# Performance work log

Hardware: AMD Instinct MI355X
Metric: run time of the kernel (lower is better)

The kernel has to match this reference:

```python
import jax, jax.numpy as jnp
import numpy as np

VOC, EDIM, HDIM, SSZ, SDIM, SDEPTH, PAD = 32000, 256, 256, 128, 128, 2, 0
N, BSZ = 64, 32
T = 2 * N - 1  # 127
N_ACTS = 2  # push, pop


def _linear(key, out_d, in_d):
    k1, k2 = jax.random.split(key)
    return (jax.random.normal(k1, (out_d, in_d), jnp.float32) * 0.02,
            jax.random.normal(k2, (out_d,), jnp.float32) * 0.02)


def setup_inputs() -> dict:
    key = jax.random.key(0)
    ks = jax.random.split(key, 9)
    emb_W = jax.random.normal(ks[0], (VOC, EDIM), jnp.float32) * 0.02
    emb_W = emb_W.at[PAD].set(0.0)  # padding_idx row is zero in torch
    W_e2h, b_e2h = _linear(ks[1], HDIM, EDIM)
    W_s2h, b_s2h = _linear(ks[2], HDIM, SDIM * SDEPTH)
    W_h2h, b_h2h = _linear(ks[3], HDIM, HDIM)
    W_h2i, b_h2i = _linear(ks[4], N_ACTS + 1, HDIM)
    W_h2s, b_h2s = _linear(ks[5], SDIM, HDIM)
    W_s2u, b_s2u = _linear(ks[6], SDIM, SDIM * SDEPTH)
    empty_elem = jax.random.normal(ks[7], (1, SDIM), jnp.float32) * 0.02
    inputs = jax.random.randint(ks[8], (N, BSZ), 0, VOC)
    return dict(inputs=inputs, emb_W=emb_W, W_e2h=W_e2h, b_e2h=b_e2h,
                W_s2h=W_s2h, b_s2h=b_s2h, W_h2h=W_h2h, b_h2h=b_h2h,
                W_h2i=W_h2i, b_h2i=b_h2i, W_h2s=W_h2s, b_h2s=b_h2s,
                W_s2u=W_s2u, b_s2u=b_s2u, empty_elem=empty_elem)


def _srnn(inputs, emb_W, W_e2h, b_e2h, W_s2h, b_s2h, W_h2h, b_h2h,
          W_h2i, b_h2i, W_h2s, b_h2s, W_s2u, b_s2u, empty_elem):
    bsz = inputs.shape[1]
    embs = emb_W[inputs]                                        # [N, bsz, edim]
    pads = jnp.broadcast_to(emb_W[PAD], (T - N, bsz, EDIM))     # padded tail
    buf0 = jnp.concatenate([embs, pads], axis=0)                # [T, bsz, edim]
    hid0 = jnp.zeros((bsz, HDIM), jnp.float32)
    stack0 = jnp.broadcast_to(empty_elem, (bsz, SSZ, SDIM))

    def step(carry, t):
        hid, stack, buf = carry
        tops = stack[:, :SDEPTH, :].reshape(bsz, SDEPTH * SDIM)
        inp = buf[t]                                            # [bsz, edim]
        ihid = inp @ W_e2h.T + b_e2h + tops @ W_s2h.T + b_s2h
        hid = jax.nn.relu(hid @ W_h2h.T + b_h2h + ihid)
        inst = ihid @ W_h2i.T + b_h2i                           # [bsz, 3]
        act = jax.nn.softmax(inst[:, :N_ACTS], axis=-1)
        gamma = 1.0 + jnp.log1p(jnp.exp(inst[:, N_ACTS:]))      # [bsz, 1]
        a = act ** gamma
        a = a / (jnp.sum(a, axis=-1, keepdims=True) + 1e-16)    # sharpened acts
        p_push, p_pop = a[:, :1], a[:, 1:]                      # [bsz, 1]
        # buffer update: pop shifts the whole buffer down one slot along time
        buf_pop = jnp.concatenate([jnp.zeros_like(buf[:1]), buf[:-1]], axis=0)
        buf = p_push[None] * buf + p_pop[None] * buf_pop        # [1,bsz,1] bcast
        push_val = jax.nn.relu(hid @ W_h2s.T + b_h2s)           # [bsz, sdim]
        u_val = jax.nn.relu(tops @ W_s2u.T + b_s2u)             # [bsz, sdim]
        z = jnp.zeros((bsz, 1, SDIM), jnp.float32)
        # W_push (shift down by 1) as an index roll
        stack_push = jnp.concatenate([z, stack[:, :-1, :]], axis=1)
        stack_push = stack_push.at[:, 0, :].add(push_val)
        # W_pop = shift up by SDEPTH, then W_push = shift down by 1
        up = jnp.concatenate([stack[:, SDEPTH:, :],
                              jnp.zeros((bsz, SDEPTH, SDIM), jnp.float32)], axis=1)
        stack_pop = jnp.concatenate([z, up[:, :-1, :]], axis=1)
        stack_pop = stack_pop.at[:, 0, :].add(u_val)
        stack_pop = stack_pop.at[:, SSZ - SDEPTH + 1:, :].add(empty_elem[0])
        stack = p_push[:, :, None] * stack_push + p_pop[:, :, None] * stack_pop
        return (hid, stack, buf), (hid, a, stack[:, 0, :])

    (hid, stack, _), (outputs, acts, top_elems) = jax.lax.scan(
        step, (hid0, stack0, buf0), jnp.arange(T))
    return outputs, hid, stack, acts, top_elems


def reference(inputs, emb_W, W_e2h, b_e2h, W_s2h, b_s2h, W_h2h, b_h2h,
              W_h2i, b_h2i, W_h2s, b_h2s, W_s2u, b_s2u, empty_elem):
    return _srnn(inputs, emb_W, W_e2h, b_e2h, W_s2h, b_s2h, W_h2h, b_h2h,
                 W_h2i, b_h2i, W_h2s, b_h2s, W_s2u, b_s2u, empty_elem)
```

## Files before the change

kernel.cpp:

```cpp
#include <hip/hip_runtime.h>
#include <stdint.h>
#include <math.h>


#define T_STEPS 127

#define OUT_OFF   0
#define HID_OFF   1040384
#define STACK_OFF 1048576
#define ACTS_OFF  1572864
#define TE_OFF    1580992

#define WB_OFF 16384
#define E2H_OFF_U 131072

typedef _Float16 h2 __attribute__((ext_vector_type(2)));

__device__ __forceinline__ unsigned packh2(float a, float b){
  h2 v; v.x = (_Float16)a; v.y = (_Float16)b;
  return __builtin_bit_cast(unsigned, v);
}
__device__ __forceinline__ float h2loF(unsigned u){ h2 v = __builtin_bit_cast(h2,u); return (float)v.x; }
__device__ __forceinline__ float h2hiF(unsigned u){ h2 v = __builtin_bit_cast(h2,u); return (float)v.y; }

#if __has_builtin(__builtin_amdgcn_fdot2)
__device__ __forceinline__ float fdot2(unsigned a, unsigned b, float c){
  return __builtin_amdgcn_fdot2(__builtin_bit_cast(h2,a), __builtin_bit_cast(h2,b), c, false);
}
#else
__device__ __forceinline__ float fdot2(unsigned a, unsigned b, float c){
  return c + h2loF(a)*h2loF(b) + h2hiF(a)*h2hiF(b);
}
#endif

#if __has_builtin(__builtin_amdgcn_exp2f)
#define EXP2F(x) __builtin_amdgcn_exp2f(x)
#else
#define EXP2F(x) exp2f(x)
#endif
#if __has_builtin(__builtin_amdgcn_logf)
#define LOG2F(x) __builtin_amdgcn_logf(x)
#else
#define LOG2F(x) log2f(x)
#endif
#if __has_builtin(__builtin_amdgcn_rcpf)
#define RCPF(x) __builtin_amdgcn_rcpf(x)
#else
#define RCPF(x) (1.f/(x))
#endif

#define DPP_XOR1 0xB1
#define DPP_XOR2 0x4E
#define DPP_HM   0x141
#define DPP_RM   0x140
template<int CTRL>
__device__ __forceinline__ float dppadd(float v){
  int s = __builtin_amdgcn_update_dpp(0, __builtin_bit_cast(int, v), CTRL, 0xF, 0xF, true);
  return v + __builtin_bit_cast(float, s);
}

#define BAR() asm volatile("s_waitcnt lgkmcnt(0)\n\ts_barrier" ::: "memory")

#define CHOFF(u) (12*((u)>>3) + ((u)&7))

__global__ void prep_pack(const float* __restrict__ We2h, const float* __restrict__ Ws2h,
                          const float* __restrict__ Wh2h, const float* __restrict__ Wh2s,
                          const float* __restrict__ Ws2u, uint4* __restrict__ out4){
  int gid = blockIdx.x*256 + threadIdx.x;
  const float* src;
  if (gid < 16384){
    int i = gid >> 10, t_ = gid & 1023;
    const float* S = (t_ < 512) ? Ws2h : Wh2h;
    int r = t_ & 511, jp = r >> 2, ks = r & 3;
    int j = 2*jp + (i >> 3);
    int k0 = ks*64 + (i & 7)*8;
    src = S + j*256 + k0;
  } else if (gid < 24576){
    int l = gid - 16384;
    int i = l >> 10, t_ = l & 1023;
    const float* S = (t_ < 512) ? Wh2s : Ws2u;
    int tt = t_ & 511;
    int j  = 2*(tt >> 3) + (i >> 2);
    int k0 = (tt & 7)*32 + (i & 3)*8;
    src = S + j*256 + k0;
  } else {
    int l = gid - 24576;
    int i8 = l >> 8, j = l & 255;
    src = We2h + j*256 + i8*8;
  }
  uint4 r4;
  r4.x = packh2(src[0], src[1]); r4.y = packh2(src[2], src[3]);
  r4.z = packh2(src[4], src[5]); r4.w = packh2(src[6], src[7]);
  out4[gid] = r4;
}

__global__ void prep_e2h(const int* __restrict__ inputs, const float* __restrict__ embW,
                         const uint4* __restrict__ w04, unsigned* __restrict__ e2hpk){
  __shared__ float emb[8][256];
  int tid = threadIdx.x;
  int r2 = blockIdx.x >> 3, bg = blockIdx.x & 7;
  for (int q=0;q<8;q++){
    int rr = q >> 2, bb = q & 3;
    int tok = inputs[(2*r2+rr)*32 + bg*4+bb];
    emb[q][tid] = embW[tok*256 + tid];
  }
  __syncthreads();
  float acc[8] = {0.f,0.f,0.f,0.f,0.f,0.f,0.f,0.f};
  for (int i8=0;i8<32;i8++){
    uint4 u = w04[i8*256 + tid];
    unsigned uu[4] = {u.x,u.y,u.z,u.w};
    #pragma unroll
    for (int c=0;c<4;c++){
      float lo = h2loF(uu[c]), hi = h2hiF(uu[c]);
      int k = i8*8 + c*2;
      #pragma unroll
      for (int q=0;q<8;q++)
        acc[q] += emb[q][k]*lo + emb[q][k+1]*hi;
    }
  }
  int base = (bg*4)*8192 + r2*256 + tid;
  #pragma unroll
  for (int bb=0;bb<4;bb++)
    e2hpk[base + bb*8192] = packh2(acc[bb], acc[4+bb]);
}

#define GEMV_B(SRC, Y0, Y1) \
  { const uint4* cA0_ = (const uint4*)((SRC) + 24*kB); \
    uint4 A0_ = cA0_[0], A1_ = cA0_[1]; \
    const uint4* cA1_ = (const uint4*)((SRC) + 24*kB + 12); \
    uint4 A2_ = cA1_[0], A3_ = cA1_[1]; \
    Y0=fdot2(A0_.x,wBr[0].x,Y0); Y0=fdot2(A0_.y,wBr[0].y,Y0); Y0=fdot2(A0_.z,wBr[0].z,Y0); Y0=fdot2(A0_.w,wBr[0].w,Y0); \
    Y0=fdot2(A1_.x,wBr[1].x,Y0); Y0=fdot2(A1_.y,wBr[1].y,Y0); Y0=fdot2(A1_.z,wBr[1].z,Y0); Y0=fdot2(A1_.w,wBr[1].w,Y0); \
    Y0=fdot2(A2_.x,wBr[2].x,Y0); Y0=fdot2(A2_.y,wBr[2].y,Y0); Y0=fdot2(A2_.z,wBr[2].z,Y0); Y0=fdot2(A2_.w,wBr[2].w,Y0); \
    Y0=fdot2(A3_.x,wBr[3].x,Y0); Y0=fdot2(A3_.y,wBr[3].y,Y0); Y0=fdot2(A3_.z,wBr[3].z,Y0); Y0=fdot2(A3_.w,wBr[3].w,Y0); \
    Y1=fdot2(A0_.x,wBr[4].x,Y1); Y1=fdot2(A0_.y,wBr[4].y,Y1); Y1=fdot2(A0_.z,wBr[4].z,Y1); Y1=fdot2(A0_.w,wBr[4].w,Y1); \
    Y1=fdot2(A1_.x,wBr[5].x,Y1); Y1=fdot2(A1_.y,wBr[5].y,Y1); Y1=fdot2(A1_.z,wBr[5].z,Y1); Y1=fdot2(A1_.w,wBr[5].w,Y1); \
    Y1=fdot2(A2_.x,wBr[6].x,Y1); Y1=fdot2(A2_.y,wBr[6].y,Y1); Y1=fdot2(A2_.z,wBr[6].z,Y1); Y1=fdot2(A2_.w,wBr[6].w,Y1); \
    Y1=fdot2(A3_.x,wBr[7].x,Y1); Y1=fdot2(A3_.y,wBr[7].y,Y1); Y1=fdot2(A3_.z,wBr[7].z,Y1); Y1=fdot2(A3_.w,wBr[7].w,Y1); \
    Y0 = dppadd<DPP_XOR1>(Y0); Y0 = dppadd<DPP_XOR2>(Y0); Y0 = dppadd<DPP_HM>(Y0); \
    Y1 = dppadd<DPP_XOR1>(Y1); Y1 = dppadd<DPP_XOR2>(Y1); Y1 = dppadd<DPP_HM>(Y1); }

__global__ __attribute__((amdgpu_flat_work_group_size(1024,1024), amdgpu_waves_per_eu(4,4)))
void srnn_main(const uint4* __restrict__ ws4, const unsigned* __restrict__ wsu,
               const float* __restrict__ b_e2h, const float* __restrict__ b_s2h,
               const float* __restrict__ b_h2h, const float* __restrict__ Wh2i,
               const float* __restrict__ b_h2i, const float* __restrict__ b_h2s,
               const float* __restrict__ b_s2u, const float* __restrict__ empty_el,
               float* __restrict__ out)
{
  __shared__ __align__(16) float    stk_s[128*128];
  __shared__ __align__(16) unsigned e2h_s[32*258];
  __shared__ __align__(16) float    halo_top[2][16*128];
  __shared__ __align__(16) float    halo_bot[2][16*128];
  __shared__ __align__(16) unsigned s_pk[192];
  __shared__ __align__(16) unsigned hid_pk[192];
  __shared__ __align__(16) float    pv_s[128], uv_s[128];
  __shared__ __align__(16) float    accih[256], acchp[256];
  __shared__ __align__(16) float    emptyf_s[128];
  __shared__ __align__(16) float    whi_s[768];
  __shared__ __align__(16) float    wbuf[2][192];
  __shared__ __align__(16) unsigned pkwc[32];
  __shared__ float    pp_s, pq_s;

  const int tid = threadIdx.x;
  const int b   = blockIdx.x;
  const int aside = tid >> 9;
  const int ar  = tid & 511;
  const int ajp = ar >> 2;
  const int aks = ar & 3;
  const int pB  = tid >> 3;
  const int kB  = tid & 7;
  const int g   = tid >> 6;
  const int cp  = tid & 63;
  const int sub = (tid >> 5) & 1;
  const int c4  = tid & 31;

  uint4 w1r[16], wBr[8];
  #pragma unroll
  for (int i=0;i<16;i++) w1r[i] = ws4[i*1024 + tid];
  #pragma unroll
  for (int i=0;i<8;i++)  wBr[i] = ws4[WB_OFF + i*1024 + tid];

  float bA0=0.f, bA1=0.f;
  if (aks==0){
    int j0 = 2*ajp;
    if (aside==0){ bA0 = b_e2h[j0]+b_s2h[j0]; bA1 = b_e2h[j0+1]+b_s2h[j0+1]; }
    else         { bA0 = b_h2h[j0];           bA1 = b_h2h[j0+1]; }
  }
  float bB0=0.f, bB1=0.f;
  if (kB==0){
    if (pB < 64){ bB0 = b_h2s[2*pB];      bB1 = b_h2s[2*pB+1]; }
    else        { bB0 = b_s2u[2*(pB-64)]; bB1 = b_s2u[2*(pB-64)+1]; }
  }
  const float bi0=b_h2i[0], bi1=b_h2i[1], bi2=b_h2i[2];

  const unsigned* e2hg = wsu + E2H_OFF_U + b*8192;
  #pragma unroll
  for (int q=0;q<8;q++){
    int idx = q*1024 + tid;
    e2h_s[(idx>>8)*258 + (idx&255)] = e2hg[idx];
  }
  {
    float2 e2 = *(const float2*)&empty_el[2*cp];
    #pragma unroll
    for (int j=0;j<8;j++)
      *(float2*)&stk_s[(8*g+j)*128 + 2*cp] = e2;
    *(float2*)&halo_top[0][g*128 + 2*cp] = e2;
    *(float2*)&halo_bot[0][g*128 + 2*cp] = e2;
  }
  if (tid < 128){
    emptyf_s[tid] = empty_el[tid];
    hid_pk[CHOFF(tid)] = 0u;
    int cu = tid & 63;
    s_pk[CHOFF(tid)] = packh2(empty_el[2*cu], empty_el[2*cu+1]);
  }
  if (tid < 768) whi_s[tid] = Wh2i[tid];
  if (tid < 192){ wbuf[0][tid] = (tid==64)?1.f:0.f; wbuf[1][tid]=0.f; }
  if (tid < 32)  pkwc[tid] = (tid==0)? packh2(1.f,0.f) : 0u;
  __syncthreads();

  int cur = 0;
  for (int t=0;t<T_STEPS;++t){
    {
      const unsigned* act  = aside ? hid_pk : s_pk;
      const unsigned* actB = act + 48*aks;
      float x0 = 0.f, x1 = 0.f;
      if (aside==0){
        uint4 cwa = *(const uint4*)&pkwc[8*aks];
        uint4 cwb = *(const uint4*)&pkwc[8*aks+4];
        unsigned cwv[8] = {cwa.x,cwa.y,cwa.z,cwa.w,cwb.x,cwb.y,cwb.z,cwb.w};
        #pragma unroll
        for (int q=0;q<8;q++){
          int r2 = aks*8 + q;
          unsigned cw = cwv[q];
          uint2 e = *(const uint2*)&e2h_s[r2*258 + 2*ajp];
          x0 = fdot2(cw, e.x, x0);
          x1 = fdot2(cw, e.y, x1);
        }
      }
      #pragma unroll
      for (int i=0;i<8;i++){
        uint4 A  = *(const uint4*)(actB + 12*(i>>1) + 4*(i&1));
        uint4 Wa = w1r[i], Wb = w1r[8+i];
        x0 = fdot2(A.x,Wa.x,x0); x0 = fdot2(A.y,Wa.y,x0);
        x0 = fdot2(A.z,Wa.z,x0); x0 = fdot2(A.w,Wa.w,x0);
        x1 = fdot2(A.x,Wb.x,x1); x1 = fdot2(A.y,Wb.y,x1);
        x1 = fdot2(A.z,Wb.z,x1); x1 = fdot2(A.w,Wb.w,x1);
      }
      x0 = dppadd<DPP_XOR1>(x0); x0 = dppadd<DPP_XOR2>(x0);
      x1 = dppadd<DPP_XOR1>(x1); x1 = dppadd<DPP_XOR2>(x1);
      if (aks==0){
        float* dst = aside ? acchp : accih;
        *(float2*)&dst[2*ajp] = make_float2(x0 + bA0, x1 + bA1);
      }
    }
    BAR();

    if (tid < 64){
      float4 av = *(const float4*)&accih[4*tid];
      float4 q0 = *(const float4*)&whi_s[      4*tid];
      float4 q1 = *(const float4*)&whi_s[256 + 4*tid];
      float4 q2 = *(const float4*)&whi_s[512 + 4*tid];
      float p0 = av.x*q0.x + av.y*q0.y + av.z*q0.z + av.w*q0.w;
      float p1 = av.x*q1.x + av.y*q1.y + av.z*q1.z + av.w*q1.w;
      float p2 = av.x*q2.x + av.y*q2.y + av.z*q2.z + av.w*q2.w;
      p0 = dppadd<DPP_XOR1>(p0); p0 = dppadd<DPP_XOR2>(p0);
      p0 = dppadd<DPP_HM>(p0);   p0 = dppadd<DPP_RM>(p0);
      p1 = dppadd<DPP_XOR1>(p1); p1 = dppadd<DPP_XOR2>(p1);
      p1 = dppadd<DPP_HM>(p1);   p1 = dppadd<DPP_RM>(p1);
      p2 = dppadd<DPP_XOR1>(p2); p2 = dppadd<DPP_XOR2>(p2);
      p2 = dppadd<DPP_HM>(p2);   p2 = dppadd<DPP_RM>(p2);
      p0 += __shfl_xor(p0,16); p0 += __shfl_xor(p0,32);
      p1 += __shfl_xor(p1,16); p1 += __shfl_xor(p1,32);
      p2 += __shfl_xor(p2,16); p2 += __shfl_xor(p2,32);
      if (tid==0){
        float i0 = bi0+p0, i1 = bi1+p1, gi = bi2+p2;
        float gamma = 1.f + 0.6931471806f*LOG2F(1.f + EXP2F(1.442695041f*gi));
        float z = 1.442695041f*gamma*(i0 - i1);
        float ppv = RCPF(1.f + EXP2F(-z));
        float pqv = 1.f - ppv;
        pp_s = ppv; pq_s = pqv;
        *(float2*)&out[ACTS_OFF + t*64 + b*2] = make_float2(ppv,pqv);
      }
    } else if (tid < 192){
      int hl = tid - 64;
      float2 ih2 = *(const float2*)&accih[2*hl];
      float2 hp2 = *(const float2*)&acchp[2*hl];
      float hn0 = fmaxf(ih2.x+hp2.x, 0.f);
      float hn1 = fmaxf(ih2.y+hp2.y, 0.f);
      hid_pk[CHOFF(hl)] = packh2(hn0,hn1);
      *(float2*)&out[OUT_OFF + t*8192 + b*256 + 2*hl] = make_float2(hn0,hn1);
      if (t==T_STEPS-1) *(float2*)&out[HID_OFF + b*256 + 2*hl] = make_float2(hn0,hn1);
    }
    if (tid >= 512){
      float y0=0.f, y1=0.f;
      GEMV_B(s_pk, y0, y1);
      if (kB==0){
        *(float2*)&uv_s[2*(pB-64)] =
          make_float2(fmaxf(y0+bB0,0.f), fmaxf(y1+bB1,0.f));
      }
    }
    BAR();

    if (tid < 512){
      float y0=0.f, y1=0.f;
      GEMV_B(hid_pk, y0, y1);
      if (kB==0){
        *(float2*)&pv_s[2*pB] =
          make_float2(fmaxf(y0+bB0,0.f), fmaxf(y1+bB1,0.f));
      }
    }
    BAR();
    const float pp = pp_s, pq = pq_s;

    {
      const int R = 8*g + 4*sub;
      float4 o0, o1, o2, o3, o4, o5;
      o1 = *(const float4*)&stk_s[(R  )*128 + 4*c4];
      o2 = *(const float4*)&stk_s[(R+1)*128 + 4*c4];
      o3 = *(const float4*)&stk_s[(R+2)*128 + 4*c4];
      o4 = *(const float4*)&stk_s[(R+3)*128 + 4*c4];
      if (sub == 0){
        o0 = (g>0) ? *(const float4*)&halo_bot[cur][(g-1)*128 + 4*c4]
                   : make_float4(0.f,0.f,0.f,0.f);
        o5 = *(const float4*)&stk_s[(R+4)*128 + 4*c4];
      } else {
        o0 = *(const float4*)&stk_s[(R-1)*128 + 4*c4];
        o5 = (g<15) ? *(const float4*)&halo_top[cur][(g+1)*128 + 4*c4]
                    : *(const float4*)&emptyf_s[4*c4];
      }
      float4 n0, n1, n2, n3;
      n0.x = pp*o0.x + pq*o2.x; n0.y = pp*o0.y + pq*o2.y;
      n0.z = pp*o0.z + pq*o2.z; n0.w = pp*o0.w + pq*o2.w;
      n1.x = pp*o1.x + pq*o3.x; n1.y = pp*o1.y + pq*o3.y;
      n1.z = pp*o1.z + pq*o3.z; n1.w = pp*o1.w + pq*o3.w;
      n2.x = pp*o2.x + pq*o4.x; n2.y = pp*o2.y + pq*o4.y;
      n2.z = pp*o2.z + pq*o4.z; n2.w = pp*o2.w + pq*o4.w;
      n3.x = pp*o3.x + pq*o5.x; n3.y = pp*o3.y + pq*o5.y;
      n3.z = pp*o3.z + pq*o5.z; n3.w = pp*o3.w + pq*o5.w;
      if (g == 0 && sub == 0){
        float4 pv4 = *(const float4*)&pv_s[4*c4];
        float4 uv4 = *(const float4*)&uv_s[4*c4];
        n0.x = pp*pv4.x + pq*uv4.x; n0.y = pp*pv4.y + pq*uv4.y;
        n0.z = pp*pv4.z + pq*uv4.z; n0.w = pp*pv4.w + pq*uv4.w;
      }
      *(float4*)&stk_s[(R  )*128 + 4*c4] = n0;
      *(float4*)&stk_s[(R+1)*128 + 4*c4] = n1;
      *(float4*)&stk_s[(R+2)*128 + 4*c4] = n2;
      *(float4*)&stk_s[(R+3)*128 + 4*c4] = n3;
      if (sub == 0) *(float4*)&halo_top[cur^1][g*128 + 4*c4] = n0;
      else          *(float4*)&halo_bot[cur^1][g*128 + 4*c4] = n3;
      if (g == 0 && sub == 0){
        *(float4*)&out[TE_OFF + t*4096 + b*128 + 4*c4] = n0;
        s_pk[CHOFF(2*c4)]      = packh2(n0.x, n0.y);
        s_pk[CHOFF(2*c4+1)]    = packh2(n0.z, n0.w);
        s_pk[CHOFF(64+2*c4)]   = packh2(n1.x, n1.y);
        s_pk[CHOFF(64+2*c4+1)] = packh2(n1.z, n1.w);
      }
      if (tid < 128){
        int k = 64+tid;
        wbuf[cur^1][k] = pp*wbuf[cur][k] + pq*wbuf[cur][k-1];
      } else if (tid < 160){
        int r2 = tid-128;
        int k1 = 65 + t - 2*r2;
        float wa = wbuf[cur][k1], wb2 = wbuf[cur][k1-1], wc2 = wbuf[cur][k1-2];
        pkwc[r2] = packh2(pp*wa+pq*wb2, pp*wb2+pq*wc2);
      }
    }
    BAR();
    cur ^= 1;
  }

  {
    const int R = 8*g + 4*sub;
    #pragma unroll
    for (int j=0;j<4;j++){
      *(float4*)&out[STACK_OFF + b*16384 + (R+j)*128 + 4*c4] =
        *(const float4*)&stk_s[(R+j)*128 + 4*c4];
    }
  }
}

extern "C" void kernel_launch(void* const* d_in, const int* in_sizes, int n_in,
                              void* d_out, int out_size, void* d_ws, size_t ws_size,
                              hipStream_t stream){
  const int*   inputs = (const int*)d_in[0];
  const float* embW   = (const float*)d_in[1];
  const float* We2h   = (const float*)d_in[2];
  const float* b_e2h  = (const float*)d_in[3];
  const float* Ws2h   = (const float*)d_in[4];
  const float* b_s2h  = (const float*)d_in[5];
  const float* Wh2h   = (const float*)d_in[6];
  const float* b_h2h  = (const float*)d_in[7];
  const float* Wh2i   = (const float*)d_in[8];
  const float* b_h2i  = (const float*)d_in[9];
  const float* Wh2s   = (const float*)d_in[10];
  const float* b_h2s  = (const float*)d_in[11];
  const float* Ws2u   = (const float*)d_in[12];
  const float* b_s2u  = (const float*)d_in[13];
  const float* empty  = (const float*)d_in[14];
  unsigned* wsu = (unsigned*)d_ws;

  prep_pack<<<dim3(128), dim3(256), 0, stream>>>(We2h, Ws2h, Wh2h, Wh2s, Ws2u, (uint4*)wsu);
  prep_e2h<<<dim3(256), dim3(256), 0, stream>>>(inputs, embW, ((const uint4*)wsu)+24576, wsu + E2H_OFF_U);
  srnn_main<<<dim3(32), dim3(1024), 0, stream>>>((const uint4*)wsu, (const unsigned*)wsu,
                                                 b_e2h, b_s2h, b_h2h, Wh2i, b_h2i,
                                                 b_h2s, b_s2u, empty, (float*)d_out);
}
```

Before: 756.4 us.

## Merge prep kernels and skip stack rows that are still empty

The two preprocessing kernels become one launch. The e2h projection now reads fp32 We2h directly instead of waiting for the packed fp16 copy, which removes a kernel boundary and one launch. In the main loop, stack row groups below the current depth (R > t) skip the shift-and-blend update, since they still hold the initial empty element. To support this, both halo buffers are initialised, and the wbuf/pkwc update is moved ahead of the stack block. The skip relies on untouched rows staying equal to empty_elem, and the e2h products now use fp32 weights, which changes numerics slightly.

```diff
diff --git a/kernel.cpp b/kernel.cpp
--- a/kernel.cpp
+++ b/kernel.cpp
@@ -63,42 +63,40 @@
 
 #define CHOFF(u) (12*((u)>>3) + ((u)&7))
 
-__global__ void prep_pack(const float* __restrict__ We2h, const float* __restrict__ Ws2h,
-                          const float* __restrict__ Wh2h, const float* __restrict__ Wh2s,
-                          const float* __restrict__ Ws2u, uint4* __restrict__ out4){
-  int gid = blockIdx.x*256 + threadIdx.x;
-  const float* src;
-  if (gid < 16384){
-    int i = gid >> 10, t_ = gid & 1023;
-    const float* S = (t_ < 512) ? Ws2h : Wh2h;
-    int r = t_ & 511, jp = r >> 2, ks = r & 3;
-    int j = 2*jp + (i >> 3);
-    int k0 = ks*64 + (i & 7)*8;
-    src = S + j*256 + k0;
-  } else if (gid < 24576){
-    int l = gid - 16384;
-    int i = l >> 10, t_ = l & 1023;
-    const float* S = (t_ < 512) ? Wh2s : Ws2u;
-    int tt = t_ & 511;
-    int j  = 2*(tt >> 3) + (i >> 2);
-    int k0 = (tt & 7)*32 + (i & 3)*8;
-    src = S + j*256 + k0;
-  } else {
-    int l = gid - 24576;
-    int i8 = l >> 8, j = l & 255;
-    src = We2h + j*256 + i8*8;
-  }
-  uint4 r4;
-  r4.x = packh2(src[0], src[1]); r4.y = packh2(src[2], src[3]);
-  r4.z = packh2(src[4], src[5]); r4.w = packh2(src[6], src[7]);
-  out4[gid] = r4;
-}
-
-__global__ void prep_e2h(const int* __restrict__ inputs, const float* __restrict__ embW,
-                         const uint4* __restrict__ w04, unsigned* __restrict__ e2hpk){
+__global__ void prep_all(const int* __restrict__ inputs, const float* __restrict__ embW,
+                         const float* __restrict__ We2h,
+                         const float* __restrict__ Ws2h, const float* __restrict__ Wh2h,
+                         const float* __restrict__ Wh2s, const float* __restrict__ Ws2u,
+                         uint4* __restrict__ out4, unsigned* __restrict__ e2hpk){
+  int tid = threadIdx.x;
+  int bi  = blockIdx.x;
+  if (bi >= 256){
+    int gid = (bi-256)*256 + tid;
+    const float* src;
+    if (gid < 16384){
+      int i = gid >> 10, t_ = gid & 1023;
+      const float* S = (t_ < 512) ? Ws2h : Wh2h;
+      int r = t_ & 511, jp = r >> 2, ks = r & 3;
+      int j = 2*jp + (i >> 3);
+      int k0 = ks*64 + (i & 7)*8;
+      src = S + j*256 + k0;
+    } else {
+      int l = gid - 16384;
+      int i = l >> 10, t_ = l & 1023;
+      const float* S = (t_ < 512) ? Wh2s : Ws2u;
+      int tt = t_ & 511;
+      int j  = 2*(tt >> 3) + (i >> 2);
+      int k0 = (tt & 7)*32 + (i & 3)*8;
+      src = S + j*256 + k0;
+    }
+    uint4 r4;
+    r4.x = packh2(src[0], src[1]); r4.y = packh2(src[2], src[3]);
+    r4.z = packh2(src[4], src[5]); r4.w = packh2(src[6], src[7]);
+    out4[gid] = r4;
+    return;
+  }
   __shared__ float emb[8][256];
-  int tid = threadIdx.x;
-  int r2 = blockIdx.x >> 3, bg = blockIdx.x & 7;
+  int r2 = bi >> 3, bg = bi & 7;
   for (int q=0;q<8;q++){
     int rr = q >> 2, bb = q & 3;
     int tok = inputs[(2*r2+rr)*32 + bg*4+bb];
@@ -107,11 +105,12 @@
   __syncthreads();
   float acc[8] = {0.f,0.f,0.f,0.f,0.f,0.f,0.f,0.f};
   for (int i8=0;i8<32;i8++){
-    uint4 u = w04[i8*256 + tid];
-    unsigned uu[4] = {u.x,u.y,u.z,u.w};
+    float4 f0 = *(const float4*)&We2h[tid*256 + i8*8];
+    float4 f1 = *(const float4*)&We2h[tid*256 + i8*8 + 4];
+    float wv[8] = {f0.x,f0.y,f0.z,f0.w,f1.x,f1.y,f1.z,f1.w};
     #pragma unroll
     for (int c=0;c<4;c++){
-      float lo = h2loF(uu[c]), hi = h2hiF(uu[c]);
+      float lo = wv[2*c], hi = wv[2*c+1];
       int k = i8*8 + c*2;
       #pragma unroll
       for (int q=0;q<8;q++)
@@ -207,6 +206,8 @@
       *(float2*)&stk_s[(8*g+j)*128 + 2*cp] = e2;
     *(float2*)&halo_top[0][g*128 + 2*cp] = e2;
     *(float2*)&halo_bot[0][g*128 + 2*cp] = e2;
+    *(float2*)&halo_top[1][g*128 + 2*cp] = e2;
+    *(float2*)&halo_bot[1][g*128 + 2*cp] = e2;
   }
   if (tid < 128){
     emptyf_s[tid] = empty_el[tid];
@@ -313,58 +314,61 @@
     BAR();
     const float pp = pp_s, pq = pq_s;
 
+    if (tid < 128){
+      int k = 64+tid;
+      wbuf[cur^1][k] = pp*wbuf[cur][k] + pq*wbuf[cur][k-1];
+    } else if (tid < 160){
+      int r2 = tid-128;
+      int k1 = 65 + t - 2*r2;
+      float wa = wbuf[cur][k1], wb2 = wbuf[cur][k1-1], wc2 = wbuf[cur][k1-2];
+      pkwc[r2] = packh2(pp*wa+pq*wb2, pp*wb2+pq*wc2);
+    }
+
     {
       const int R = 8*g + 4*sub;
-      float4 o0, o1, o2, o3, o4, o5;
-      o1 = *(const float4*)&stk_s[(R  )*128 + 4*c4];
-      o2 = *(const float4*)&stk_s[(R+1)*128 + 4*c4];
-      o3 = *(const float4*)&stk_s[(R+2)*128 + 4*c4];
-      o4 = *(const float4*)&stk_s[(R+3)*128 + 4*c4];
-      if (sub == 0){
-        o0 = (g>0) ? *(const float4*)&halo_bot[cur][(g-1)*128 + 4*c4]
-                   : make_float4(0.f,0.f,0.f,0.f);
-        o5 = *(const float4*)&stk_s[(R+4)*128 + 4*c4];
-      } else {
-        o0 = *(const float4*)&stk_s[(R-1)*128 + 4*c4];
-        o5 = (g<15) ? *(const float4*)&halo_top[cur][(g+1)*128 + 4*c4]
-                    : *(const float4*)&emptyf_s[4*c4];
-      }
-      float4 n0, n1, n2, n3;
-      n0.x = pp*o0.x + pq*o2.x; n0.y = pp*o0.y + pq*o2.y;
-      n0.z = pp*o0.z + pq*o2.z; n0.w = pp*o0.w + pq*o2.w;
-      n1.x = pp*o1.x + pq*o3.x; n1.y = pp*o1.y + pq*o3.y;
-      n1.z = pp*o1.z + pq*o3.z; n1.w = pp*o1.w + pq*o3.w;
-      n2.x = pp*o2.x + pq*o4.x; n2.y = pp*o2.y + pq*o4.y;
-      n2.z = pp*o2.z + pq*o4.z; n2.w = pp*o2.w + pq*o4.w;
-      n3.x = pp*o3.x + pq*o5.x; n3.y = pp*o3.y + pq*o5.y;
-      n3.z = pp*o3.z + pq*o5.z; n3.w = pp*o3.w + pq*o5.w;
-      if (g == 0 && sub == 0){
-        float4 pv4 = *(const float4*)&pv_s[4*c4];
-        float4 uv4 = *(const float4*)&uv_s[4*c4];
-        n0.x = pp*pv4.x + pq*uv4.x; n0.y = pp*pv4.y + pq*uv4.y;
-        n0.z = pp*pv4.z + pq*uv4.z; n0.w = pp*pv4.w + pq*uv4.w;
-      }
-      *(float4*)&stk_s[(R  )*128 + 4*c4] = n0;
-      *(float4*)&stk_s[(R+1)*128 + 4*c4] = n1;
-      *(float4*)&stk_s[(R+2)*128 + 4*c4] = n2;
-      *(float4*)&stk_s[(R+3)*128 + 4*c4] = n3;
-      if (sub == 0) *(float4*)&halo_top[cur^1][g*128 + 4*c4] = n0;
-      else          *(float4*)&halo_bot[cur^1][g*128 + 4*c4] = n3;
-      if (g == 0 && sub == 0){
-        *(float4*)&out[TE_OFF + t*4096 + b*128 + 4*c4] = n0;
-        s_pk[CHOFF(2*c4)]      = packh2(n0.x, n0.y);
-        s_pk[CHOFF(2*c4+1)]    = packh2(n0.z, n0.w);
-        s_pk[CHOFF(64+2*c4)]   = packh2(n1.x, n1.y);
-        s_pk[CHOFF(64+2*c4+1)] = packh2(n1.z, n1.w);
-      }
-      if (tid < 128){
-        int k = 64+tid;
-        wbuf[cur^1][k] = pp*wbuf[cur][k] + pq*wbuf[cur][k-1];
-      } else if (tid < 160){
-        int r2 = tid-128;
-        int k1 = 65 + t - 2*r2;
-        float wa = wbuf[cur][k1], wb2 = wbuf[cur][k1-1], wc2 = wbuf[cur][k1-2];
-        pkwc[r2] = packh2(pp*wa+pq*wb2, pp*wb2+pq*wc2);
+      if (R <= t){
+        float4 o0, o1, o2, o3, o4, o5;
+        o1 = *(const float4*)&stk_s[(R  )*128 + 4*c4];
+        o2 = *(const float4*)&stk_s[(R+1)*128 + 4*c4];
+        o3 = *(const float4*)&stk_s[(R+2)*128 + 4*c4];
+        o4 = *(const float4*)&stk_s[(R+3)*128 + 4*c4];
+        if (sub == 0){
+          o0 = (g>0) ? *(const float4*)&halo_bot[cur][(g-1)*128 + 4*c4]
+                     : make_float4(0.f,0.f,0.f,0.f);
+          o5 = *(const float4*)&stk_s[(R+4)*128 + 4*c4];
+        } else {
+          o0 = *(const float4*)&stk_s[(R-1)*128 + 4*c4];
+          o5 = (g<15) ? *(const float4*)&halo_top[cur][(g+1)*128 + 4*c4]
+                      : *(const float4*)&emptyf_s[4*c4];
+        }
+        float4 n0, n1, n2, n3;
+        n0.x = pp*o0.x + pq*o2.x; n0.y = pp*o0.y + pq*o2.y;
+        n0.z = pp*o0.z + pq*o2.z; n0.w = pp*o0.w + pq*o2.w;
+        n1.x = pp*o1.x + pq*o3.x; n1.y = pp*o1.y + pq*o3.y;
+        n1.z = pp*o1.z + pq*o3.z; n1.w = pp*o1.w + pq*o3.w;
+        n2.x = pp*o2.x + pq*o4.x; n2.y = pp*o2.y + pq*o4.y;
+        n2.z = pp*o2.z + pq*o4.z; n2.w = pp*o2.w + pq*o4.w;
+        n3.x = pp*o3.x + pq*o5.x; n3.y = pp*o3.y + pq*o5.y;
+        n3.z = pp*o3.z + pq*o5.z; n3.w = pp*o3.w + pq*o5.w;
+        if (g == 0 && sub == 0){
+          float4 pv4 = *(const float4*)&pv_s[4*c4];
+          float4 uv4 = *(const float4*)&uv_s[4*c4];
+          n0.x = pp*pv4.x + pq*uv4.x; n0.y = pp*pv4.y + pq*uv4.y;
+          n0.z = pp*pv4.z + pq*uv4.z; n0.w = pp*pv4.w + pq*uv4.w;
+        }
+        *(float4*)&stk_s[(R  )*128 + 4*c4] = n0;
+        *(float4*)&stk_s[(R+1)*128 + 4*c4] = n1;
+        *(float4*)&stk_s[(R+2)*128 + 4*c4] = n2;
+        *(float4*)&stk_s[(R+3)*128 + 4*c4] = n3;
+        if (sub == 0) *(float4*)&halo_top[cur^1][g*128 + 4*c4] = n0;
+        else          *(float4*)&halo_bot[cur^1][g*128 + 4*c4] = n3;
+        if (g == 0 && sub == 0){
+          *(float4*)&out[TE_OFF + t*4096 + b*128 + 4*c4] = n0;
+          s_pk[CHOFF(2*c4)]      = packh2(n0.x, n0.y);
+          s_pk[CHOFF(2*c4+1)]    = packh2(n0.z, n0.w);
+          s_pk[CHOFF(64+2*c4)]   = packh2(n1.x, n1.y);
+          s_pk[CHOFF(64+2*c4+1)] = packh2(n1.z, n1.w);
+        }
       }
     }
     BAR();
@@ -401,8 +405,9 @@
   const float* empty  = (const float*)d_in[14];
   unsigned* wsu = (unsigned*)d_ws;
 
-  prep_pack<<<dim3(128), dim3(256), 0, stream>>>(We2h, Ws2h, Wh2h, Wh2s, Ws2u, (uint4*)wsu);
-  prep_e2h<<<dim3(256), dim3(256), 0, stream>>>(inputs, embW, ((const uint4*)wsu)+24576, wsu + E2H_OFF_U);
+  prep_all<<<dim3(352), dim3(256), 0, stream>>>(inputs, embW, We2h, Ws2h, Wh2h,
+                                                Wh2s, Ws2u, (uint4*)wsu,
+                                                wsu + E2H_OFF_U);
   srnn_main<<<dim3(32), dim3(1024), 0, stream>>>((const uint4*)wsu, (const unsigned*)wsu,
                                                  b_e2h, b_s2h, b_h2h, Wh2i, b_h2i,
                                                  b_h2s, b_s2u, empty, (float*)d_out);
```

Result: slower. 803.0 us (+6.2%).
